# Performance work log

Hardware: AMD Instinct MI355X
Metric: run time of the kernel (lower is better)

The kernel has to match this reference:

```python
import jax, jax.numpy as jnp
import numpy as np

NEG_SLOPE = 0.2
EPS = 1e-16


def _gat_layer(x, src, dst, W, a_src, a_dst, b, n_nodes):
    # x: [N, Fin], W: [Fout, Fin]; src/dst: [E'] (self-loops already appended)
    h = x @ W.T                              # [N, Fout]
    alpha_s = h @ a_src                      # [N] per-source score
    alpha_d = h @ a_dst                      # [N] per-dest score
    e = jax.nn.leaky_relu(alpha_s[src] + alpha_d[dst], NEG_SLOPE)  # [E']
    # segment softmax over destination nodes (PyG softmax semantics)
    m = jax.ops.segment_max(e, dst, num_segments=n_nodes)          # [N]
    ex = jnp.exp(e - m[dst])                                       # [E']
    s = jax.ops.segment_sum(ex, dst, num_segments=n_nodes)         # [N]
    alpha = ex / (s[dst] + EPS)                                    # [E']
    out = jax.ops.segment_sum(alpha[:, None] * h[src], dst, num_segments=n_nodes)
    return out + b, alpha


def setup_inputs() -> dict:
    key = jax.random.key(0)
    ks = jax.random.split(key, 14)
    N, E, F_IN, H1, H2, F_OUT = 50000, 800000, 128, 64, 64, 32
    sc = 0.1
    return {
        "x": jax.random.normal(ks[0], (N, F_IN), dtype=jnp.float32),
        "edge_index": jax.random.randint(ks[1], (2, E), 0, N, dtype=jnp.int64),
        "W1": jax.random.normal(ks[2], (H1, F_IN), dtype=jnp.float32) * sc,
        "a_src1": jax.random.normal(ks[3], (H1,), dtype=jnp.float32) * sc,
        "a_dst1": jax.random.normal(ks[4], (H1,), dtype=jnp.float32) * sc,
        "b1": jnp.zeros((H1,), dtype=jnp.float32),
        "W2": jax.random.normal(ks[5], (H2, H1), dtype=jnp.float32) * sc,
        "a_src2": jax.random.normal(ks[6], (H2,), dtype=jnp.float32) * sc,
        "a_dst2": jax.random.normal(ks[7], (H2,), dtype=jnp.float32) * sc,
        "b2": jnp.zeros((H2,), dtype=jnp.float32),
        "W3": jax.random.normal(ks[8], (F_OUT, H2), dtype=jnp.float32) * sc,
        "a_src3": jax.random.normal(ks[9], (F_OUT,), dtype=jnp.float32) * sc,
        "a_dst3": jax.random.normal(ks[10], (F_OUT,), dtype=jnp.float32) * sc,
        "b3": jnp.zeros((F_OUT,), dtype=jnp.float32),
    }


def reference(x, edge_index, W1, a_src1, a_dst1, b1, W2, a_src2, a_dst2, b2, W3, a_src3, a_dst3, b3):
    N = x.shape[0]
    loops = jnp.arange(N, dtype=edge_index.dtype)
    src = jnp.concatenate([edge_index[0], loops])  # add_self_loops=True
    dst = jnp.concatenate([edge_index[1], loops])

    h, alpha1 = _gat_layer(x, src, dst, W1, a_src1, a_dst1, b1, N)
    h = jax.nn.relu(h)
    h, _ = _gat_layer(h, src, dst, W2, a_src2, a_dst2, b2, N)
    h = jax.nn.relu(h)
    out, _ = _gat_layer(h, src, dst, W3, a_src3, a_dst3, b3, N)
    # att_tuple = (edge_index with self loops, attention coefficients of layer 1)
    return (jnp.stack([src, dst]), alpha1, out)
```

## Files before the change

kernel.cpp:

```cpp
#include <hip/hip_runtime.h>
#include <hip/hip_bf16.h>
#include <math.h>

#define NEG_SLOPE 0.2f
#define GAT_EPS 1e-16f

constexpr int NN = 50000;
constexpr int NE = 800000;
constexpr int EP = NE + NN;
constexpr int NB = (NN + 255) / 256;

__device__ inline void edge_sd(const int* __restrict__ ei, int i, int& s, int& d) {
    if (i < NE) { s = ei[i]; d = ei[NE + i]; }
    else        { s = d = i - NE; }
}

__device__ inline float bflo(unsigned int h) { return __uint_as_float(h << 16); }
__device__ inline float bfhi(unsigned int h) { return __uint_as_float(h & 0xffff0000u); }

__global__ void k_edges_hist(const int* __restrict__ ei, float* __restrict__ out0,
                             unsigned int* __restrict__ cntp,
                             unsigned short* __restrict__ rank) {
    int i = blockIdx.x * blockDim.x + threadIdx.x;
    if (i >= EP) return;
    int s, d; edge_sd(ei, i, s, d);
    __builtin_nontemporal_store((float)s, &out0[i]);
    __builtin_nontemporal_store((float)d, &out0[EP + i]);
    unsigned int add = (d & 1) ? 0x10000u : 1u;
    unsigned int old = atomicAdd(&cntp[d >> 1], add);
    unsigned short r = (unsigned short)((d & 1) ? (old >> 16) : (old & 0xffffu));
    __builtin_nontemporal_store(r, &rank[i]);
}

__global__ void k_scan1(const unsigned int* __restrict__ cntp, int* __restrict__ rowptr,
                        int* __restrict__ bsum) {
    __shared__ int sh[256];
    int t = threadIdx.x, i = blockIdx.x * 256 + t;
    int v = 0;
    if (i < NN) {
        unsigned int pv = cntp[i >> 1];
        v = (i & 1) ? (int)(pv >> 16) : (int)(pv & 0xffffu);
    }
    sh[t] = v; __syncthreads();
    for (int off = 1; off < 256; off <<= 1) {
        int x = (t >= off) ? sh[t - off] : 0;
        __syncthreads();
        sh[t] += x;
        __syncthreads();
    }
    if (i < NN) rowptr[i] = sh[t] - v;
    if (t == 255) bsum[blockIdx.x] = sh[255];
}

__global__ void k_scan2(int* __restrict__ bsum, int* __restrict__ boff) {
    __shared__ int sh[256];
    int t = threadIdx.x;
    int v = (t < NB) ? bsum[t] : 0;
    sh[t] = v; __syncthreads();
    for (int off = 1; off < 256; off <<= 1) {
        int x = (t >= off) ? sh[t - off] : 0;
        __syncthreads();
        sh[t] += x;
        __syncthreads();
    }
    if (t < NB) boff[t] = sh[t] - v;
}

__global__ void k_scan3(int* __restrict__ rowptr, const int* __restrict__ boff) {
    int i = blockIdx.x * blockDim.x + threadIdx.x;
    if (i < NN) rowptr[i] += boff[i >> 8];
    if (i == 0) rowptr[NN] = EP;
}

__global__ void k_fill(const int* __restrict__ ei, const unsigned short* __restrict__ rank,
                       const int* __restrict__ rowptr, unsigned short* __restrict__ col) {
    int i = blockIdx.x * blockDim.x + threadIdx.x;
    if (i >= EP) return;
    int s, d; edge_sd(ei, i, s, d);
    int pos = rowptr[d] + (int)rank[i];
    col[pos] = (unsigned short)s;
}

__global__ void k_alpha_out(const int* __restrict__ ei, const float* __restrict__ as_,
                            const float* __restrict__ ad_, const float* __restrict__ inv,
                            float* __restrict__ out_alpha) {
    int i = blockIdx.x * blockDim.x + threadIdx.x;
    if (i >= EP) return;
    int s, d; edge_sd(ei, i, s, d);
    float v = as_[s] + ad_[d];
    v = v > 0.f ? v : NEG_SLOPE * v;
    __builtin_nontemporal_store(__expf(v) * inv[d], &out_alpha[i]);
}

struct alignas(8) bh4 { __hip_bfloat16 a, b, c, d; };

__device__ inline void fma4(float4& acc, float x, const float4& w) {
    acc.x = fmaf(x, w.x, acc.x);
    acc.y = fmaf(x, w.y, acc.y);
    acc.z = fmaf(x, w.z, acc.z);
    acc.w = fmaf(x, w.w, acc.w);
}

template <int FIN, int FOUT, int NPB>
__global__ __launch_bounds__(256) void k_gemm_t(const float* __restrict__ in,
                                                const float* __restrict__ W,
                                                const float* __restrict__ avs,
                                                const float* __restrict__ avd,
                                                __hip_bfloat16* __restrict__ H,
                                                float* __restrict__ as_,
                                                float* __restrict__ ad_, int n) {
    constexpr int TF = FOUT / 4;
    constexpr int XS = FIN + 4;
    constexpr int WS = FOUT + 4;
    __shared__ float sX[NPB * XS];
    __shared__ float sWt[FIN * WS];
    int tid = threadIdx.x;
    for (int idx = tid; idx < FIN * FOUT; idx += 256) {
        int f = idx % FOUT, k = idx / FOUT;
        sWt[k * WS + f] = W[f * FIN + k];
    }
    int nb = blockIdx.x * NPB;
    for (int idx = tid; idx < NPB * (FIN / 4); idx += 256) {
        int node = idx / (FIN / 4), kq = idx % (FIN / 4);
        int g = nb + node;
        float4 v = make_float4(0.f, 0.f, 0.f, 0.f);
        if (g < n) v = *(const float4*)&in[(size_t)g * FIN + kq * 4];
        *(float4*)&sX[node * XS + kq * 4] = v;
    }
    __syncthreads();

    int fq = tid % TF, ng = tid / TF;
    int n0 = ng * 4;
    float4 acc0 = make_float4(0.f, 0.f, 0.f, 0.f);
    float4 acc1 = acc0, acc2 = acc0, acc3 = acc0;
    for (int k = 0; k < FIN; k += 4) {
        float4 w0 = *(const float4*)&sWt[(k + 0) * WS + fq * 4];
        float4 w1 = *(const float4*)&sWt[(k + 1) * WS + fq * 4];
        float4 w2 = *(const float4*)&sWt[(k + 2) * WS + fq * 4];
        float4 w3 = *(const float4*)&sWt[(k + 3) * WS + fq * 4];
        float4 x0 = *(const float4*)&sX[(n0 + 0) * XS + k];
        float4 x1 = *(const float4*)&sX[(n0 + 1) * XS + k];
        float4 x2 = *(const float4*)&sX[(n0 + 2) * XS + k];
        float4 x3 = *(const float4*)&sX[(n0 + 3) * XS + k];
        fma4(acc0, x0.x, w0); fma4(acc0, x0.y, w1); fma4(acc0, x0.z, w2); fma4(acc0, x0.w, w3);
        fma4(acc1, x1.x, w0); fma4(acc1, x1.y, w1); fma4(acc1, x1.z, w2); fma4(acc1, x1.w, w3);
        fma4(acc2, x2.x, w0); fma4(acc2, x2.y, w1); fma4(acc2, x2.z, w2); fma4(acc2, x2.w, w3);
        fma4(acc3, x3.x, w0); fma4(acc3, x3.y, w1); fma4(acc3, x3.z, w2); fma4(acc3, x3.w, w3);
    }
    float4 accs[4] = {acc0, acc1, acc2, acc3};
    float4 vs4 = *(const float4*)&avs[fq * 4];
    float4 vd4 = *(const float4*)&avd[fq * 4];
#pragma unroll
    for (int j = 0; j < 4; ++j) {
        int g = nb + n0 + j;
        float ps = accs[j].x * vs4.x + accs[j].y * vs4.y + accs[j].z * vs4.z + accs[j].w * vs4.w;
        float pd = accs[j].x * vd4.x + accs[j].y * vd4.y + accs[j].z * vd4.z + accs[j].w * vd4.w;
#pragma unroll
        for (int off = TF / 2; off; off >>= 1) {
            ps += __shfl_down(ps, off, TF);
            pd += __shfl_down(pd, off, TF);
        }
        if (g < n) {
            if (fq == 0) { as_[g] = ps; ad_[g] = pd; }
            bh4 o;
            o.a = __float2bfloat16(accs[j].x);
            o.b = __float2bfloat16(accs[j].y);
            o.c = __float2bfloat16(accs[j].z);
            o.d = __float2bfloat16(accs[j].w);
            *(bh4*)&H[(size_t)g * FOUT + fq * 4] = o;
        }
    }
}

template <int FOUT, bool RELU, bool WRITE_INV>
__global__ __launch_bounds__(256) void k_node_attn(
    const int* __restrict__ rowptr, const unsigned short* __restrict__ col,
    const float* __restrict__ as_, const float* __restrict__ ad_,
    const __hip_bfloat16* __restrict__ H, const float* __restrict__ bias,
    float* __restrict__ outp, float* __restrict__ inv_out) {
    int wid = (blockIdx.x * blockDim.x + threadIdx.x) >> 6;
    int lane = threadIdx.x & 63;
    if (wid >= NN) return;
    int start = rowptr[wid], end = rowptr[wid + 1];
    float adv = ad_[wid];
    const unsigned int* __restrict__ H2 = (const unsigned int*)H;

    float sloc = 0.f;
    float ax = 0.f, ay = 0.f;
    for (int c = start; c < end; c += 64) {
        int e = c + lane;
        float p = 0.f;
        int sc = 0;
        if (e < end) {
            sc = (int)col[e];
            float v = as_[sc] + adv;
            v = v > 0.f ? v : NEG_SLOPE * v;
            p = __expf(v);
        }
        sloc += p;
        int cnt = end - c; if (cnt > 64) cnt = 64;
        if (FOUT == 64) {
            int half = lane >> 5, fl = lane & 31;
            int j = 0;
            for (; j + 16 <= cnt; j += 16) {
                float pp[8]; int ss[8]; unsigned int hh[8];
#pragma unroll
                for (int k = 0; k < 8; ++k) {
                    int ek = j + 2 * k + half;
                    pp[k] = __shfl(p, ek);
                    ss[k] = __shfl(sc, ek);
                }
#pragma unroll
                for (int k = 0; k < 8; ++k) hh[k] = H2[((size_t)ss[k] << 5) + fl];
#pragma unroll
                for (int k = 0; k < 8; ++k) {
                    ax = fmaf(pp[k], bflo(hh[k]), ax);
                    ay = fmaf(pp[k], bfhi(hh[k]), ay);
                }
            }
            for (; j + 8 <= cnt; j += 8) {
                int e0 = j + half, e1 = j + 2 + half, e2 = j + 4 + half, e3 = j + 6 + half;
                float p0 = __shfl(p, e0), p1 = __shfl(p, e1);
                float p2 = __shfl(p, e2), p3 = __shfl(p, e3);
                int s0 = __shfl(sc, e0), s1 = __shfl(sc, e1);
                int s2 = __shfl(sc, e2), s3 = __shfl(sc, e3);
                unsigned int h0 = H2[((size_t)s0 << 5) + fl];
                unsigned int h1 = H2[((size_t)s1 << 5) + fl];
                unsigned int h2 = H2[((size_t)s2 << 5) + fl];
                unsigned int h3 = H2[((size_t)s3 << 5) + fl];
                ax = fmaf(p0, bflo(h0), ax); ay = fmaf(p0, bfhi(h0), ay);
                ax = fmaf(p1, bflo(h1), ax); ay = fmaf(p1, bfhi(h1), ay);
                ax = fmaf(p2, bflo(h2), ax); ay = fmaf(p2, bfhi(h2), ay);
                ax = fmaf(p3, bflo(h3), ax); ay = fmaf(p3, bfhi(h3), ay);
            }
            for (; j < cnt; j += 2) {
                int e0 = j + half;
                float p0 = __shfl(p, e0);
                int   s0 = __shfl(sc, e0);
                unsigned int h0 = H2[((size_t)s0 << 5) + fl];
                ax = fmaf(p0, bflo(h0), ax); ay = fmaf(p0, bfhi(h0), ay);
            }
        } else {
            int q = lane >> 4, fl = lane & 15;
            int j = 0;
            for (; j + 16 <= cnt; j += 16) {
                int e0 = j + q, e1 = j + 4 + q, e2 = j + 8 + q, e3 = j + 12 + q;
                float p0 = __shfl(p, e0), p1 = __shfl(p, e1);
                float p2 = __shfl(p, e2), p3 = __shfl(p, e3);
                int s0 = __shfl(sc, e0), s1 = __shfl(sc, e1);
                int s2 = __shfl(sc, e2), s3 = __shfl(sc, e3);
                unsigned int h0 = H2[((size_t)s0 << 4) + fl];
                unsigned int h1 = H2[((size_t)s1 << 4) + fl];
                unsigned int h2 = H2[((size_t)s2 << 4) + fl];
                unsigned int h3 = H2[((size_t)s3 << 4) + fl];
                ax = fmaf(p0, bflo(h0), ax); ay = fmaf(p0, bfhi(h0), ay);
                ax = fmaf(p1, bflo(h1), ax); ay = fmaf(p1, bfhi(h1), ay);
                ax = fmaf(p2, bflo(h2), ax); ay = fmaf(p2, bfhi(h2), ay);
                ax = fmaf(p3, bflo(h3), ax); ay = fmaf(p3, bfhi(h3), ay);
            }
            for (; j < cnt; j += 4) {
                int e0 = j + q;
                float p0 = __shfl(p, e0);
                int   s0 = __shfl(sc, e0);
                unsigned int h0 = H2[((size_t)s0 << 4) + fl];
                ax = fmaf(p0, bflo(h0), ax); ay = fmaf(p0, bfhi(h0), ay);
            }
        }
    }
    for (int off = 32; off; off >>= 1) sloc += __shfl_xor(sloc, off);
    float inv = 1.f / (sloc + GAT_EPS);
    if (WRITE_INV && lane == 0) inv_out[wid] = inv;

    if (FOUT == 64) {
        ax += __shfl_xor(ax, 32);
        ay += __shfl_xor(ay, 32);
        if (lane < 32) {
            float2 bb = *(const float2*)&bias[lane * 2];
            float o0 = bb.x + ax * inv;
            float o1 = bb.y + ay * inv;
            if (RELU) { o0 = fmaxf(o0, 0.f); o1 = fmaxf(o1, 0.f); }
            *(float2*)&outp[((size_t)wid << 6) + lane * 2] = make_float2(o0, o1);
        }
    } else {
        ax += __shfl_xor(ax, 32); ay += __shfl_xor(ay, 32);
        ax += __shfl_xor(ax, 16); ay += __shfl_xor(ay, 16);
        if (lane < 16) {
            float2 bb = *(const float2*)&bias[lane * 2];
            float o0 = bb.x + ax * inv;
            float o1 = bb.y + ay * inv;
            if (RELU) { o0 = fmaxf(o0, 0.f); o1 = fmaxf(o1, 0.f); }
            *(float2*)&outp[((size_t)wid << 5) + lane * 2] = make_float2(o0, o1);
        }
    }
}

extern "C" void kernel_launch(void* const* d_in, const int* in_sizes, int n_in,
                              void* d_out, int out_size, void* d_ws, size_t ws_size,
                              hipStream_t stream) {
    const float* x  = (const float*)d_in[0];
    const int*   ei = (const int*)d_in[1];
    const float* W1 = (const float*)d_in[2];
    const float* as1 = (const float*)d_in[3];
    const float* ad1 = (const float*)d_in[4];
    const float* b1 = (const float*)d_in[5];
    const float* W2 = (const float*)d_in[6];
    const float* as2 = (const float*)d_in[7];
    const float* ad2 = (const float*)d_in[8];
    const float* b2 = (const float*)d_in[9];
    const float* W3 = (const float*)d_in[10];
    const float* as3 = (const float*)d_in[11];
    const float* ad3 = (const float*)d_in[12];
    const float* b3 = (const float*)d_in[13];

    float* out = (float*)d_out;
    float* out_edges = out;
    float* out_alpha = out + 2 * EP;
    float* out_final = out + 3 * EP;

    char* w = (char*)d_ws;
    size_t o = 0;
    float* as_ = (float*)(w + o); o += (size_t)NN * 4;
    float* ad_ = (float*)(w + o); o += (size_t)NN * 4;
    float* inv = (float*)(w + o); o += (size_t)NN * 4;
    __hip_bfloat16* H = (__hip_bfloat16*)(w + o); o += (size_t)NN * 64 * 2;
    int* rowptr = (int*)(w + o); o += ((size_t)(NN + 1) * 4 + 15) & ~15ull;
    unsigned int* cntp = (unsigned int*)(w + o); o += (size_t)(NN / 2) * 4;
    unsigned short* rank = (unsigned short*)(w + o); o += (size_t)EP * 2;
    unsigned short* col  = (unsigned short*)(w + o); o += (size_t)EP * 2;
    int* bsum   = (int*)(w + o); o += 1024;
    int* boff   = (int*)(w + o); o += 1024;
    const size_t aggBytes = (size_t)NN * 64 * 4;
    float* agg = (ws_size >= o + aggBytes)
        ? (float*)(w + o)
        : (float*)d_in[0];

    hipMemsetAsync(cntp, 0, (size_t)(NN / 2) * 4, stream);
    k_edges_hist<<<(EP + 255) / 256, 256, 0, stream>>>(ei, out_edges, cntp, rank);
    k_scan1<<<NB, 256, 0, stream>>>(cntp, rowptr, bsum);
    k_scan2<<<1, 256, 0, stream>>>(bsum, boff);
    k_scan3<<<NB, 256, 0, stream>>>(rowptr, boff);
    k_fill<<<(EP + 255) / 256, 256, 0, stream>>>(ei, rank, rowptr, col);

    const int nblk = (NN * 64 + 255) / 256;

    k_gemm_t<128, 64, 64><<<(NN + 63) / 64, 256, 0, stream>>>(x, W1, as1, ad1, H, as_, ad_, NN);
    k_node_attn<64, true, true><<<nblk, 256, 0, stream>>>(rowptr, col, as_, ad_, H, b1,
                                                          agg, inv);
    k_alpha_out<<<(EP + 255) / 256, 256, 0, stream>>>(ei, as_, ad_, inv, out_alpha);

    k_gemm_t<64, 64, 64><<<(NN + 63) / 64, 256, 0, stream>>>(agg, W2, as2, ad2, H, as_, ad_, NN);
    k_node_attn<64, true, false><<<nblk, 256, 0, stream>>>(rowptr, col, as_, ad_, H, b2,
                                                           agg, nullptr);

    k_gemm_t<64, 32, 128><<<(NN + 127) / 128, 256, 0, stream>>>(agg, W3, as3, ad3, H, as_, ad_,
                                                                NN);
    k_node_attn<32, false, false><<<nblk, 256, 0, stream>>>(rowptr, col, as_, ad_, H, b3,
                                                            out_final, nullptr);
}
```

Before: 311.6 us.

## Replace global atomic degree histogram with per-block shared-memory counting sort

Builds the CSR by giving each of 128 large blocks its own edge chunk. Each block counts destinations in a shared-memory histogram of packed 8-bit counters, then writes that histogram to global memory. A column-wise scan over the block histograms produces per-chunk offsets, and the fill step adds the row pointer, the chunk offset, the block offset and the local rank. This removes contended global atomics and shrinks the rank array to bytes. In exchange it writes and scans a 6.4 MB histogram, runs only 128 blocks, and relies on per-node in-degrees fitting in 8 bits.

```diff
diff --git a/kernel.cpp b/kernel.cpp
--- a/kernel.cpp
+++ b/kernel.cpp
@@ -10,6 +10,12 @@
 constexpr int EP = NE + NN;
 constexpr int NB = (NN + 255) / 256;
 
+constexpr int PB  = 128;
+constexpr int PT  = 1024;
+constexpr int CH  = (EP + PB - 1) / PB;
+constexpr int NCH = 4;
+constexpr int BPC = PB / NCH;
+
 __device__ inline void edge_sd(const int* __restrict__ ei, int i, int& s, int& d) {
     if (i < NE) { s = ei[i]; d = ei[NE + i]; }
     else        { s = d = i - NE; }
@@ -18,28 +24,57 @@
 __device__ inline float bflo(unsigned int h) { return __uint_as_float(h << 16); }
 __device__ inline float bfhi(unsigned int h) { return __uint_as_float(h & 0xffff0000u); }
 
-__global__ void k_edges_hist(const int* __restrict__ ei, float* __restrict__ out0,
-                             unsigned int* __restrict__ cntp,
-                             unsigned short* __restrict__ rank) {
-    int i = blockIdx.x * blockDim.x + threadIdx.x;
-    if (i >= EP) return;
-    int s, d; edge_sd(ei, i, s, d);
-    __builtin_nontemporal_store((float)s, &out0[i]);
-    __builtin_nontemporal_store((float)d, &out0[EP + i]);
-    unsigned int add = (d & 1) ? 0x10000u : 1u;
-    unsigned int old = atomicAdd(&cntp[d >> 1], add);
-    unsigned short r = (unsigned short)((d & 1) ? (old >> 16) : (old & 0xffffu));
-    __builtin_nontemporal_store(r, &rank[i]);
-}
-
-__global__ void k_scan1(const unsigned int* __restrict__ cntp, int* __restrict__ rowptr,
-                        int* __restrict__ bsum) {
+__global__ __launch_bounds__(PT) void k_p1_hist(const int* __restrict__ ei,
+                                                float* __restrict__ out0,
+                                                unsigned char* __restrict__ hist,
+                                                unsigned char* __restrict__ rank8) {
+    __shared__ unsigned int sh[NN / 4];
+    int b = blockIdx.x, t = threadIdx.x;
+    for (int w = t; w < NN / 4; w += PT) sh[w] = 0u;
+    __syncthreads();
+    int i0 = b * CH;
+    int iend = i0 + CH; if (iend > EP) iend = EP;
+    for (int i = i0 + t; i < iend; i += PT) {
+        int s, d; edge_sd(ei, i, s, d);
+        __builtin_nontemporal_store((float)s, &out0[i]);
+        __builtin_nontemporal_store((float)d, &out0[EP + i]);
+        int sft = (d & 3) * 8;
+        unsigned int old = atomicAdd(&sh[d >> 2], 1u << sft);
+        __builtin_nontemporal_store((unsigned char)(old >> sft), &rank8[i]);
+    }
+    __syncthreads();
+    unsigned int* hw = (unsigned int*)(hist + (size_t)b * NN);
+    for (int w = t; w < NN / 4; w += PT) hw[w] = sh[w];
+}
+
+__global__ __launch_bounds__(256) void k_p2_scan(unsigned char* __restrict__ hist,
+                                                 unsigned char* __restrict__ chunksum) {
+    int n = blockIdx.x * 256 + threadIdx.x;
+    int c = blockIdx.y;
+    if (n >= NN) return;
+    unsigned int run = 0;
+    size_t idx = (size_t)(c * BPC) * NN + n;
+    for (int b = 0; b < BPC; ++b, idx += NN) {
+        unsigned int v = hist[idx];
+        hist[idx] = (unsigned char)run;
+        run += v;
+    }
+    chunksum[n * NCH + c] = (unsigned char)run;
+}
+
+__global__ void k_scan1(const unsigned char* __restrict__ chunksum,
+                        unsigned char* __restrict__ chunkoff,
+                        int* __restrict__ rowptr, int* __restrict__ bsum) {
     __shared__ int sh[256];
     int t = threadIdx.x, i = blockIdx.x * 256 + t;
     int v = 0;
     if (i < NN) {
-        unsigned int pv = cntp[i >> 1];
-        v = (i & 1) ? (int)(pv >> 16) : (int)(pv & 0xffffu);
+        unsigned int cs = *(const unsigned int*)&chunksum[i * 4];
+        unsigned int c0 = cs & 0xffu, c1 = (cs >> 8) & 0xffu;
+        unsigned int c2 = (cs >> 16) & 0xffu, c3 = cs >> 24;
+        unsigned int o1 = c0, o2 = c0 + c1, o3 = c0 + c1 + c2;
+        *(unsigned int*)&chunkoff[i * 4] = (o1 << 8) | (o2 << 16) | (o3 << 24);
+        v = (int)(o3 + c3);
     }
     sh[t] = v; __syncthreads();
     for (int off = 1; off < 256; off <<= 1) {
@@ -72,13 +107,22 @@
     if (i == 0) rowptr[NN] = EP;
 }
 
-__global__ void k_fill(const int* __restrict__ ei, const unsigned short* __restrict__ rank,
-                       const int* __restrict__ rowptr, unsigned short* __restrict__ col) {
-    int i = blockIdx.x * blockDim.x + threadIdx.x;
-    if (i >= EP) return;
-    int s, d; edge_sd(ei, i, s, d);
-    int pos = rowptr[d] + (int)rank[i];
-    col[pos] = (unsigned short)s;
+__global__ __launch_bounds__(PT) void k_fill(const int* __restrict__ ei,
+                                             const unsigned char* __restrict__ rank8,
+                                             const unsigned char* __restrict__ hist,
+                                             const unsigned char* __restrict__ chunkoff,
+                                             const int* __restrict__ rowptr,
+                                             unsigned short* __restrict__ col) {
+    int b = blockIdx.x, t = threadIdx.x;
+    int c = b / BPC;
+    const unsigned char* __restrict__ hrow = hist + (size_t)b * NN;
+    int i0 = b * CH;
+    int iend = i0 + CH; if (iend > EP) iend = EP;
+    for (int i = i0 + t; i < iend; i += PT) {
+        int s, d; edge_sd(ei, i, s, d);
+        int pos = rowptr[d] + (int)chunkoff[d * 4 + c] + (int)hrow[d] + (int)rank8[i];
+        col[pos] = (unsigned short)s;
+    }
 }
 
 __global__ void k_alpha_out(const int* __restrict__ ei, const float* __restrict__ as_,
@@ -319,27 +363,34 @@
 
     char* w = (char*)d_ws;
     size_t o = 0;
-    float* as_ = (float*)(w + o); o += (size_t)NN * 4;
-    float* ad_ = (float*)(w + o); o += (size_t)NN * 4;
-    float* inv = (float*)(w + o); o += (size_t)NN * 4;
-    __hip_bfloat16* H = (__hip_bfloat16*)(w + o); o += (size_t)NN * 64 * 2;
-    int* rowptr = (int*)(w + o); o += ((size_t)(NN + 1) * 4 + 15) & ~15ull;
-    unsigned int* cntp = (unsigned int*)(w + o); o += (size_t)(NN / 2) * 4;
-    unsigned short* rank = (unsigned short*)(w + o); o += (size_t)EP * 2;
-    unsigned short* col  = (unsigned short*)(w + o); o += (size_t)EP * 2;
-    int* bsum   = (int*)(w + o); o += 1024;
-    int* boff   = (int*)(w + o); o += 1024;
-    const size_t aggBytes = (size_t)NN * 64 * 4;
+    auto alloc = [&](size_t bytes) { void* p = w + o; o = (o + bytes + 15) & ~15ull; return p; };
+    float* as_ = (float*)alloc((size_t)NN * 4);
+    float* ad_ = (float*)alloc((size_t)NN * 4);
+    float* inv = (float*)alloc((size_t)NN * 4);
+    __hip_bfloat16* H = (__hip_bfloat16*)alloc((size_t)NN * 64 * 2);
+    int* rowptr = (int*)alloc((size_t)(NN + 1) * 4);
+    unsigned char* rank8 = (unsigned char*)alloc((size_t)EP);
+    unsigned short* col  = (unsigned short*)alloc((size_t)EP * 2);
+    unsigned char* chunksum = (unsigned char*)alloc((size_t)NN * 4);
+    unsigned char* chunkoff = (unsigned char*)alloc((size_t)NN * 4);
+    int* bsum = (int*)alloc(1024);
+    int* boff = (int*)alloc(1024);
+
+    const size_t aggBytes  = (size_t)NN * 64 * 4;
+    const size_t histBytes = (size_t)PB * NN;
     float* agg = (ws_size >= o + aggBytes)
         ? (float*)(w + o)
         : (float*)d_in[0];
-
-    hipMemsetAsync(cntp, 0, (size_t)(NN / 2) * 4, stream);
-    k_edges_hist<<<(EP + 255) / 256, 256, 0, stream>>>(ei, out_edges, cntp, rank);
-    k_scan1<<<NB, 256, 0, stream>>>(cntp, rowptr, bsum);
+    unsigned char* hist = (ws_size >= o + aggBytes + histBytes)
+        ? (unsigned char*)(w + o + aggBytes)
+        : (unsigned char*)out_final;
+
+    k_p1_hist<<<PB, PT, 0, stream>>>(ei, out_edges, hist, rank8);
+    k_p2_scan<<<dim3(NB, NCH), 256, 0, stream>>>(hist, chunksum);
+    k_scan1<<<NB, 256, 0, stream>>>(chunksum, chunkoff, rowptr, bsum);
     k_scan2<<<1, 256, 0, stream>>>(bsum, boff);
     k_scan3<<<NB, 256, 0, stream>>>(rowptr, boff);
-    k_fill<<<(EP + 255) / 256, 256, 0, stream>>>(ei, rank, rowptr, col);
+    k_fill<<<PB, PT, 0, stream>>>(ei, rank8, hist, chunkoff, rowptr, col);
 
     const int nblk = (NN * 64 + 255) / 256;
 
```

Result: faster. 304.2 us (-2.4%).
